# Kernel optimization log

Measured on AMD Instinct MI355X. Metric: run time of the kernel, lower is better.

Reference implementation:

```python
import jax, jax.numpy as jnp
import numpy as np

B, S, C, H, D = 4, 2048, 512, 8, 64
EPS = 1e-5
SCALE = D ** -0.5


def layer_norm(x, w, b):
    m = jnp.mean(x, axis=-1, keepdims=True)
    v = jnp.var(x, axis=-1, keepdims=True)
    return (x - m) * jax.lax.rsqrt(v + EPS) * w + b


def setup_inputs() -> dict:
    key = jax.random.key(0)
    ks = jax.random.split(key, 7)
    s = 0.02
    return {
        "x": jax.random.normal(ks[0], (B, S, C), jnp.float32),
        "Wq": jax.random.normal(ks[1], (C, H * D), jnp.float32) * s,
        "Wk": jax.random.normal(ks[2], (C, H * D), jnp.float32) * s,
        "Wv": jax.random.normal(ks[3], (C, H * D), jnp.float32) * s,
        "Wo": jax.random.normal(ks[4], (H * D, C), jnp.float32) * s,
        "ln1_w": jnp.ones((C,), jnp.float32), "ln1_b": jnp.zeros((C,), jnp.float32),
        "ff_ln1_w": jnp.ones((C,), jnp.float32), "ff_ln1_b": jnp.zeros((C,), jnp.float32),
        "ff_w1": jax.random.normal(ks[5], (C, C), jnp.float32) * s, "ff_b1": jnp.zeros((C,), jnp.float32),
        "ff_ln2_w": jnp.ones((C,), jnp.float32), "ff_ln2_b": jnp.zeros((C,), jnp.float32),
        "ff_w2": jax.random.normal(ks[6], (C, C), jnp.float32) * s, "ff_b2": jnp.zeros((C,), jnp.float32),
        "ln2_w": jnp.ones((C,), jnp.float32), "ln2_b": jnp.zeros((C,), jnp.float32),
    }


def causal_attention(x, Wq, Wk, Wv, Wo):
    # Mathematically identical to the bucketed memory-efficient attention:
    # online-softmax bucketing changes compute order, not the result.
    q = (x @ Wq).reshape(B, S, H, D).transpose(0, 2, 1, 3)  # [B,H,S,D]
    k = (x @ Wk).reshape(B, S, H, D).transpose(0, 2, 1, 3)
    v = (x @ Wv).reshape(B, S, H, D).transpose(0, 2, 1, 3)
    scores = jnp.einsum('bhqd,bhkd->bhqk', q, k) * SCALE  # [B,H,S,S]
    causal = jnp.tril(jnp.ones((S, S), bool))
    scores = jnp.where(causal, scores, jnp.finfo(scores.dtype).min)
    attn = jax.nn.softmax(scores, axis=-1)
    out = jnp.einsum('bhqk,bhkd->bhqd', attn, v)
    out = out.transpose(0, 2, 1, 3).reshape(B, S, H * D)
    return out @ Wo


def reference(x, Wq, Wk, Wv, Wo, ln1_w, ln1_b, ff_ln1_w, ff_ln1_b, ff_w1, ff_b1,
              ff_ln2_w, ff_ln2_b, ff_w2, ff_b2, ln2_w, ln2_b):
    a = causal_attention(x, Wq, Wk, Wv, Wo)
    x_ln = layer_norm(a + x, ln1_w, ln1_b)
    h = layer_norm(x_ln, ff_ln1_w, ff_ln1_b) @ ff_w1 + ff_b1
    h = layer_norm(h, ff_ln2_w, ff_ln2_b) @ ff_w2 + ff_b2
    return layer_norm(h + x_ln, ln2_w, ln2_b)
```

## Files before the change

### kernel.cpp

```cpp
#include <hip/hip_runtime.h>

#define B_ 4
#define S_ 2048
#define C_ 512
#define H_ 8
#define D_ 64
#define M_ 8192

typedef short s8v __attribute__((ext_vector_type(8)));
typedef short s4v __attribute__((ext_vector_type(4)));
typedef float f4v __attribute__((ext_vector_type(4)));
typedef unsigned short u16;
typedef unsigned int u32;
typedef u32 u2v __attribute__((ext_vector_type(2)));

__device__ __forceinline__ u16 f2b(float f) {
    u32 u = __builtin_bit_cast(u32, f);
    u = u + 0x7fffu + ((u >> 16) & 1u);
    return (u16)(u >> 16);
}

__device__ __forceinline__ void b2f8(const s8v v, float* f) {
    #pragma unroll
    for (int k = 0; k < 8; ++k)
        f[k] = __builtin_bit_cast(float, (u32)(u16)v[k] << 16);
}

__device__ __forceinline__ void gl2lds16(const void* g, void* l) {
    __builtin_amdgcn_global_load_lds(
        (const __attribute__((address_space(1))) void*)g,
        (__attribute__((address_space(3))) void*)l, 16, 0, 0);
}

__device__ __forceinline__ s4v pk4(float a, float b, float c, float d) {
    u32 w0, w1;
    asm("v_cvt_pk_bf16_f32 %0, %1, %2" : "=v"(w0) : "v"(a), "v"(b));
    asm("v_cvt_pk_bf16_f32 %0, %1, %2" : "=v"(w1) : "v"(c), "v"(d));
    u2v t; t[0] = w0; t[1] = w1;
    return __builtin_bit_cast(s4v, t);
}

__global__ __launch_bounds__(256) void prep_k(const float* __restrict__ x,
                                              u16* __restrict__ xb,
                                              const float* __restrict__ s0,
                                              const float* __restrict__ s1,
                                              const float* __restrict__ s2,
                                              const float* __restrict__ s3,
                                              const float* __restrict__ s4,
                                              const float* __restrict__ s5,
                                              u16* __restrict__ d0,
                                              u16* __restrict__ d1,
                                              u16* __restrict__ d2,
                                              u16* __restrict__ d3,
                                              u16* __restrict__ d4,
                                              u16* __restrict__ d5)
{
    __shared__ float t[32][33];
    const int bx = blockIdx.x;
    if (bx < 4096) {
        const int i = (bx * 256 + (int)threadIdx.x) * 4;
        const float4 v = *(const float4*)&x[i];
        ushort4 o;
        o.x = f2b(v.x); o.y = f2b(v.y); o.z = f2b(v.z); o.w = f2b(v.w);
        *(ushort4*)&xb[i] = o;
        return;
    }
    const int tb = bx - 4096;
    const int z = tb >> 8, rem = tb & 255;
    const float* W; u16* Wt;
    switch (z) {
        case 0: W = s0; Wt = d0; break;
        case 1: W = s1; Wt = d1; break;
        case 2: W = s2; Wt = d2; break;
        case 3: W = s3; Wt = d3; break;
        case 4: W = s4; Wt = d4; break;
        default: W = s5; Wt = d5; break;
    }
    const int tx = threadIdx.x & 31, ty = threadIdx.x >> 5;
    const int n0 = (rem & 15) * 32, k0 = (rem >> 4) * 32;
    #pragma unroll
    for (int i = 0; i < 4; ++i)
        t[ty + i * 8][tx] = W[(size_t)(k0 + ty + i * 8) * C_ + n0 + tx];
    __syncthreads();
    #pragma unroll
    for (int i = 0; i < 4; ++i)
        Wt[(size_t)(n0 + ty + i * 8) * C_ + k0 + tx] = f2b(t[tx][ty + i * 8]);
}

template <bool OB>
__global__ __launch_bounds__(256) void gemm_k(const u16* __restrict__ A,
                                              const u16* __restrict__ Bt,
                                              const float* __restrict__ bias,
                                              void* __restrict__ outv)
{
    __shared__ u16 As[2][128][64];
    __shared__ u16 Bs[2][64][64];
    const int tid = threadIdx.x;
    const int lane = tid & 63, w = tid >> 6;
    const int q4 = lane >> 4, l16 = lane & 15;
    const int wr = w >> 1, wc = w & 1;
    const int bm = blockIdx.x * 128, bn = blockIdx.y * 64;
    const int sr8  = lane >> 3;
    const int scol = ((lane & 7) ^ sr8) * 8;

    f4v acc[4][2];
    #pragma unroll
    for (int i = 0; i < 4; ++i)
        #pragma unroll
        for (int j = 0; j < 2; ++j) acc[i][j] = (f4v){0.f, 0.f, 0.f, 0.f};

    const u16* Ab = A  + (size_t)bm * C_;
    const u16* Bb = Bt + (size_t)bn * C_;

    auto stage = [&](int bf, int kt) {
        const int k0 = kt * 64;
        #pragma unroll
        for (int t = 0; t < 4; ++t)
            gl2lds16(Ab + (size_t)(w * 32 + t * 8 + sr8) * C_ + k0 + scol,
                     (char*)As + bf * 16384 + (w * 32 + t * 8) * 128);
        #pragma unroll
        for (int t = 0; t < 2; ++t)
            gl2lds16(Bb + (size_t)(w * 16 + t * 8 + sr8) * C_ + k0 + scol,
                     (char*)Bs + bf * 8192 + (w * 16 + t * 8) * 128);
    };

    stage(0, 0);
    for (int kt = 0; kt < 8; ++kt) {
        __syncthreads();
        const int bf = kt & 1;
        if (kt < 7) stage(bf ^ 1, kt + 1);
        #pragma unroll
        for (int kk = 0; kk < 2; ++kk) {
            const int pc = ((kk * 4 + q4) ^ (l16 & 7)) * 8;
            s8v a[4], b[2];
            #pragma unroll
            for (int i = 0; i < 4; ++i)
                a[i] = *(const s8v*)&As[bf][wr * 64 + i * 16 + l16][pc];
            #pragma unroll
            for (int j = 0; j < 2; ++j)
                b[j] = *(const s8v*)&Bs[bf][wc * 32 + j * 16 + l16][pc];
            #pragma unroll
            for (int i = 0; i < 4; ++i)
                #pragma unroll
                for (int j = 0; j < 2; ++j)
                    acc[i][j] = __builtin_amdgcn_mfma_f32_16x16x32_bf16(a[i], b[j], acc[i][j], 0, 0, 0);
        }
    }

    if constexpr (OB) {
        __syncthreads();
        u16* Ls = (u16*)As;
        #pragma unroll
        for (int j = 0; j < 2; ++j) {
            const int nl = wc * 32 + j * 16 + l16;
            const float bj = bias ? bias[bn + nl] : 0.0f;
            #pragma unroll
            for (int i = 0; i < 4; ++i) {
                const int ml = wr * 64 + i * 16 + q4 * 4;
                #pragma unroll
                for (int reg = 0; reg < 4; ++reg)
                    Ls[(ml + reg) * 72 + nl] = f2b(acc[i][j][reg] + bj);
            }
        }
        __syncthreads();
        #pragma unroll
        for (int pass = 0; pass < 4; ++pass) {
            const int idx = tid + pass * 256;
            const int r = idx >> 3, c = idx & 7;
            const s8v v = *(const s8v*)&Ls[r * 72 + c * 8];
            *(s8v*)&((u16*)outv)[(size_t)(bm + r) * C_ + bn + c * 8] = v;
        }
    } else {
        #pragma unroll
        for (int j = 0; j < 2; ++j) {
            const int n = bn + wc * 32 + j * 16 + l16;
            const float bj = bias ? bias[n] : 0.0f;
            #pragma unroll
            for (int i = 0; i < 4; ++i) {
                const int m = bm + wr * 64 + i * 16 + q4 * 4;
                #pragma unroll
                for (int reg = 0; reg < 4; ++reg)
                    ((float*)outv)[(size_t)(m + reg) * C_ + n] = acc[i][j][reg] + bj;
            }
        }
    }
}

__global__ __launch_bounds__(256) void qkv_k(const u16* __restrict__ A,
                                             const u16* __restrict__ Wq,
                                             const u16* __restrict__ Wk,
                                             const u16* __restrict__ Wv,
                                             u16* __restrict__ oq,
                                             u16* __restrict__ ok,
                                             u16* __restrict__ ovt)
{
    __shared__ u16 As[2][128][64];
    __shared__ u16 Bs[2][64][64];
    const int tid = threadIdx.x;
    const int lane = tid & 63, w = tid >> 6;
    const int q4 = lane >> 4, l16 = lane & 15;
    const int wr = w >> 1, wc = w & 1;
    const int nt = blockIdx.y, which = nt >> 3;
    const u16* Bt = which == 0 ? Wq : (which == 1 ? Wk : Wv);
    const int bm = blockIdx.x * 128, bn = (nt & 7) * 64;
    const int sr8  = lane >> 3;
    const int scol = ((lane & 7) ^ sr8) * 8;

    f4v acc[4][2];
    #pragma unroll
    for (int i = 0; i < 4; ++i)
        #pragma unroll
        for (int j = 0; j < 2; ++j) acc[i][j] = (f4v){0.f, 0.f, 0.f, 0.f};

    const u16* Ab = A  + (size_t)bm * C_;
    const u16* Bb = Bt + (size_t)bn * C_;

    auto stage = [&](int bf, int kt) {
        const int k0 = kt * 64;
        #pragma unroll
        for (int t = 0; t < 4; ++t)
            gl2lds16(Ab + (size_t)(w * 32 + t * 8 + sr8) * C_ + k0 + scol,
                     (char*)As + bf * 16384 + (w * 32 + t * 8) * 128);
        #pragma unroll
        for (int t = 0; t < 2; ++t)
            gl2lds16(Bb + (size_t)(w * 16 + t * 8 + sr8) * C_ + k0 + scol,
                     (char*)Bs + bf * 8192 + (w * 16 + t * 8) * 128);
    };

    stage(0, 0);
    for (int kt = 0; kt < 8; ++kt) {
        __syncthreads();
        const int bf = kt & 1;
        if (kt < 7) stage(bf ^ 1, kt + 1);
        #pragma unroll
        for (int kk = 0; kk < 2; ++kk) {
            const int pc = ((kk * 4 + q4) ^ (l16 & 7)) * 8;
            s8v a[4], b[2];
            #pragma unroll
            for (int i = 0; i < 4; ++i)
                a[i] = *(const s8v*)&As[bf][wr * 64 + i * 16 + l16][pc];
            #pragma unroll
            for (int j = 0; j < 2; ++j)
                b[j] = *(const s8v*)&Bs[bf][wc * 32 + j * 16 + l16][pc];
            #pragma unroll
            for (int i = 0; i < 4; ++i)
                #pragma unroll
                for (int j = 0; j < 2; ++j)
                    acc[i][j] = __builtin_amdgcn_mfma_f32_16x16x32_bf16(a[i], b[j], acc[i][j], 0, 0, 0);
        }
    }

    if (which < 2) {
        __syncthreads();
        u16* Ls = (u16*)As;
        #pragma unroll
        for (int j = 0; j < 2; ++j) {
            const int nl = wc * 32 + j * 16 + l16;
            #pragma unroll
            for (int i = 0; i < 4; ++i) {
                const int ml = wr * 64 + i * 16 + q4 * 4;
                #pragma unroll
                for (int reg = 0; reg < 4; ++reg)
                    Ls[(ml + reg) * 72 + nl] = f2b(acc[i][j][reg]);
            }
        }
        __syncthreads();
        u16* dst = which == 0 ? oq : ok;
        #pragma unroll
        for (int pass = 0; pass < 4; ++pass) {
            const int idx = tid + pass * 256;
            const int r = idx >> 3, c = idx & 7;
            const s8v v = *(const s8v*)&Ls[r * 72 + c * 8];
            const int cg = which == 0 ? c : ((c & ~3) | ((c & 3) ^ ((r >> 2) & 3)));
            *(s8v*)&dst[(size_t)(bm + r) * C_ + bn + cg * 8] = v;
        }
    } else {
        const int bglob = bm >> 11;
        const int sbase = bm & (S_ - 1);
        #pragma unroll
        for (int j = 0; j < 2; ++j) {
            const int n = bn + wc * 32 + j * 16 + l16;
            const int h = n >> 6, d = n & 63;
            u16* vrow = ovt + ((size_t)(bglob * H_ + h) * D_ + d) * S_;
            const int xw = d & 7;
            #pragma unroll
            for (int i = 0; i < 4; ++i) {
                const int s = sbase + wr * 64 + i * 16 + q4 * 4;
                const int pg = ((s & 31) >> 2) ^ xw;
                s4v pv;
                #pragma unroll
                for (int reg = 0; reg < 4; ++reg) pv[reg] = (short)f2b(acc[i][j][reg]);
                *(s4v*)&vrow[(s & ~31) + (pg << 2)] = pv;
            }
        }
    }
}

__global__ __launch_bounds__(256) void ln2xb_k(const u16* __restrict__ in,
                                               const float* __restrict__ res,
                                               const float* __restrict__ w1,
                                               const float* __restrict__ b1,
                                               const float* __restrict__ w2,
                                               const float* __restrict__ b2,
                                               u16* __restrict__ out1,
                                               u16* __restrict__ out2)
{
    const int lane = threadIdx.x & 63;
    const int row  = blockIdx.x * 4 + (threadIdx.x >> 6);
    const size_t off = (size_t)row * C_ + lane * 8;
    float v[8];
    b2f8(*(const s8v*)&in[off], v);
    {
        const float4 r0 = *(const float4*)&res[off];
        const float4 r1 = *(const float4*)&res[off + 4];
        v[0] += r0.x; v[1] += r0.y; v[2] += r0.z; v[3] += r0.w;
        v[4] += r1.x; v[5] += r1.y; v[6] += r1.z; v[7] += r1.w;
    }
    float s = 0.f, ss = 0.f;
    #pragma unroll
    for (int k = 0; k < 8; ++k) { s += v[k]; ss += v[k] * v[k]; }
    #pragma unroll
    for (int o = 32; o >= 1; o >>= 1) { s += __shfl_xor(s, o); ss += __shfl_xor(ss, o); }
    float mean = s * (1.0f / C_);
    float rstd = rsqrtf(ss * (1.0f / C_) - mean * mean + 1e-5f);

    const float4 wA0 = *(const float4*)&w1[lane * 8];
    const float4 wA1 = *(const float4*)&w1[lane * 8 + 4];
    const float4 bA0 = *(const float4*)&b1[lane * 8];
    const float4 bA1 = *(const float4*)&b1[lane * 8 + 4];
    const float wA[8] = {wA0.x, wA0.y, wA0.z, wA0.w, wA1.x, wA1.y, wA1.z, wA1.w};
    const float bA[8] = {bA0.x, bA0.y, bA0.z, bA0.w, bA1.x, bA1.y, bA1.z, bA1.w};
    float y[8];
    s8v o1;
    #pragma unroll
    for (int k = 0; k < 8; ++k) {
        y[k] = (v[k] - mean) * rstd * wA[k] + bA[k];
        o1[k] = (short)f2b(y[k]);
    }
    *(s8v*)&out1[off] = o1;

    s = 0.f; ss = 0.f;
    #pragma unroll
    for (int k = 0; k < 8; ++k) { s += y[k]; ss += y[k] * y[k]; }
    #pragma unroll
    for (int o = 32; o >= 1; o >>= 1) { s += __shfl_xor(s, o); ss += __shfl_xor(ss, o); }
    mean = s * (1.0f / C_);
    rstd = rsqrtf(ss * (1.0f / C_) - mean * mean + 1e-5f);

    const float4 wB0 = *(const float4*)&w2[lane * 8];
    const float4 wB1 = *(const float4*)&w2[lane * 8 + 4];
    const float4 bB0 = *(const float4*)&b2[lane * 8];
    const float4 bB1 = *(const float4*)&b2[lane * 8 + 4];
    const float wB[8] = {wB0.x, wB0.y, wB0.z, wB0.w, wB1.x, wB1.y, wB1.z, wB1.w};
    const float bB[8] = {bB0.x, bB0.y, bB0.z, bB0.w, bB1.x, bB1.y, bB1.z, bB1.w};
    s8v o2;
    #pragma unroll
    for (int k = 0; k < 8; ++k)
        o2[k] = (short)f2b((y[k] - mean) * rstd * wB[k] + bB[k]);
    *(s8v*)&out2[off] = o2;
}

__global__ __launch_bounds__(256) void lnb_k(const u16* __restrict__ in,
                                             const float* __restrict__ w,
                                             const float* __restrict__ bb,
                                             u16* __restrict__ out)
{
    const int lane = threadIdx.x & 63;
    const int row  = blockIdx.x * 4 + (threadIdx.x >> 6);
    const size_t off = (size_t)row * C_ + lane * 8;
    float v[8];
    b2f8(*(const s8v*)&in[off], v);
    float s = 0.f, ss = 0.f;
    #pragma unroll
    for (int k = 0; k < 8; ++k) { s += v[k]; ss += v[k] * v[k]; }
    #pragma unroll
    for (int o = 32; o >= 1; o >>= 1) { s += __shfl_xor(s, o); ss += __shfl_xor(ss, o); }
    const float mean = s * (1.0f / C_);
    const float rstd = rsqrtf(ss * (1.0f / C_) - mean * mean + 1e-5f);
    const float4 w0 = *(const float4*)&w[lane * 8];
    const float4 w1 = *(const float4*)&w[lane * 8 + 4];
    const float4 b0 = *(const float4*)&bb[lane * 8];
    const float4 b1 = *(const float4*)&bb[lane * 8 + 4];
    const float wv[8] = {w0.x, w0.y, w0.z, w0.w, w1.x, w1.y, w1.z, w1.w};
    const float bv[8] = {b0.x, b0.y, b0.z, b0.w, b1.x, b1.y, b1.z, b1.w};
    s8v o;
    #pragma unroll
    for (int k = 0; k < 8; ++k)
        o[k] = (short)f2b((v[k] - mean) * rstd * wv[k] + bv[k]);
    *(s8v*)&out[off] = o;
}

__global__ __launch_bounds__(256) void lnfin_k(const u16* __restrict__ in,
                                               const u16* __restrict__ res,
                                               const float* __restrict__ w,
                                               const float* __restrict__ bb,
                                               float* __restrict__ out)
{
    const int lane = threadIdx.x & 63;
    const int row  = blockIdx.x * 4 + (threadIdx.x >> 6);
    const size_t off = (size_t)row * C_ + lane * 8;
    float v[8], r[8];
    b2f8(*(const s8v*)&in[off], v);
    b2f8(*(const s8v*)&res[off], r);
    #pragma unroll
    for (int k = 0; k < 8; ++k) v[k] += r[k];
    float s = 0.f, ss = 0.f;
    #pragma unroll
    for (int k = 0; k < 8; ++k) { s += v[k]; ss += v[k] * v[k]; }
    #pragma unroll
    for (int o = 32; o >= 1; o >>= 1) { s += __shfl_xor(s, o); ss += __shfl_xor(ss, o); }
    const float mean = s * (1.0f / C_);
    const float rstd = rsqrtf(ss * (1.0f / C_) - mean * mean + 1e-5f);
    const float4 w0 = *(const float4*)&w[lane * 8];
    const float4 w1 = *(const float4*)&w[lane * 8 + 4];
    const float4 b0 = *(const float4*)&bb[lane * 8];
    const float4 b1 = *(const float4*)&bb[lane * 8 + 4];
    const float wv[8] = {w0.x, w0.y, w0.z, w0.w, w1.x, w1.y, w1.z, w1.w};
    const float bv[8] = {b0.x, b0.y, b0.z, b0.w, b1.x, b1.y, b1.z, b1.w};
    float4 o0, o1;
    o0.x = (v[0] - mean) * rstd * wv[0] + bv[0];
    o0.y = (v[1] - mean) * rstd * wv[1] + bv[1];
    o0.z = (v[2] - mean) * rstd * wv[2] + bv[2];
    o0.w = (v[3] - mean) * rstd * wv[3] + bv[3];
    o1.x = (v[4] - mean) * rstd * wv[4] + bv[4];
    o1.y = (v[5] - mean) * rstd * wv[5] + bv[5];
    o1.z = (v[6] - mean) * rstd * wv[6] + bv[6];
    o1.w = (v[7] - mean) * rstd * wv[7] + bv[7];
    *(float4*)&out[off]     = o0;
    *(float4*)&out[off + 4] = o1;
}

__global__ __launch_bounds__(512, 4) void attn_k(const u16* __restrict__ Q,
                                                 const u16* __restrict__ K,
                                                 const u16* __restrict__ Vt,
                                                 u16* __restrict__ O)
{
    __shared__ char smem[65536];
    u16* KsB = (u16*)smem;
    u16* VsB = (u16*)(smem + 32768);
    const int tid = threadIdx.x;
    const int lane = tid & 63, w = tid >> 6;
    const int grp = w >> 2, wl = w & 3;
    const int q4 = lane >> 4, l16 = lane & 15;
    const int h = blockIdx.x, px = blockIdx.y, b = blockIdx.z;
    const int qH = 31 - px, qL = px;
    const int nH = 32 - px;
    const size_t base  = ((size_t)b * S_) * C_ + h * D_;
    const size_t basev = ((size_t)(b * H_ + h)) * D_ * S_;
    const int lr = lane >> 2, lc = (lane & 3) * 8;
    const int kq = (q4 ^ ((l16 >> 2) & 3)) * 8;
    const int qrow = wl * 16 + l16;

    const u16* ksA = KsB + grp * 4096;
    const u16* ksBp = KsB + (grp + 2) * 4096;
    const u16* vsA = VsB + grp * 4096;
    const u16* vsBp = VsB + (grp + 2) * 4096;
    char* kdA = (char*)KsB + grp * 8192 + wl * 1024;
    char* kdB = (char*)KsB + (grp + 2) * 8192 + wl * 1024;
    char* vdA = (char*)VsB + grp * 8192 + wl * 1024;
    char* vdB = (char*)VsB + (grp + 2) * 8192 + wl * 1024;

    const int kfb = l16 * 32 + kq;
    int vfb[4];
    #pragma unroll
    for (int c = 0; c < 4; ++c)
        vfb[c] = l16 * 32 + ((((c & 1) * 4 + q4) ^ (l16 & 7)) * 4);

    const u16* kpt = K  + base  + (size_t)(wl * 16 + lr) * C_ + lc;
    const u16* vpt = Vt + basev + (size_t)(wl * 16 + lr) * S_ + lc;

    f4v acc[4]; float lp[4];
    f4v oH[4];  float lpH[4];
    #pragma unroll
    for (int j = 0; j < 4; ++j) {
        acc[j] = (f4v){0.f, 0.f, 0.f, 0.f}; lp[j] = 0.f;
        oH[j]  = (f4v){0.f, 0.f, 0.f, 0.f}; lpH[j] = 0.f;
    }
    s8v qf[2];
    #pragma unroll
    for (int kh = 0; kh < 2; ++kh)
        qf[kh] = *(const s8v*)&Q[base + (size_t)(qH * 64 + qrow) * C_ + kh * 32 + q4 * 8];

    bool dumped = false, wrapped = false;

    auto dumpacc = [&]() {
        #pragma unroll
        for (int j = 0; j < 4; ++j) {
            oH[j] = acc[j]; lpH[j] = lp[j];
            acc[j] = (f4v){0.f, 0.f, 0.f, 0.f}; lp[j] = 0.f;
        }
        #pragma unroll
        for (int kh = 0; kh < 2; ++kh)
            qf[kh] = *(const s8v*)&Q[base + (size_t)(qL * 64 + qrow) * C_ + kh * 32 + q4 * 8];
    };

    auto compute = [&](const u16* ks, const u16* vs, const bool diag) {
        f4v sc[4];
        #pragma unroll
        for (int j = 0; j < 4; ++j) sc[j] = (f4v){0.f, 0.f, 0.f, 0.f};
        __builtin_amdgcn_s_setprio(1);
        #pragma unroll
        for (int kh = 0; kh < 2; ++kh)
            #pragma unroll
            for (int j = 0; j < 4; ++j) {
                const s8v kf = *(const s8v*)&ks[kfb + kh * 2048 + j * 512];
                sc[j] = __builtin_amdgcn_mfma_f32_16x16x32_bf16(kf, qf[kh], sc[j], 0, 0, 0);
            }
        __builtin_amdgcn_s_setprio(0);
        s4v pa[4];
        if (diag) {
            #pragma unroll
            for (int j = 0; j < 4; ++j) {
                float pv[4];
                #pragma unroll
                for (int reg = 0; reg < 4; ++reg) {
                    float tt = fmaf(sc[j][reg], 0.18033688011112043f, -11.541560327111707f);
                    if ((j * 16 + q4 * 4 + reg) > qrow) tt = -128.0f;
                    pv[reg] = exp2f(tt);
                }
                lp[j] += (pv[0] + pv[1]) + (pv[2] + pv[3]);
                pa[j] = pk4(pv[0], pv[1], pv[2], pv[3]);
            }
        } else {
            #pragma unroll
            for (int j = 0; j < 4; ++j) {
                float pv[4];
                #pragma unroll
                for (int reg = 0; reg < 4; ++reg)
                    pv[reg] = exp2f(fmaf(sc[j][reg], 0.18033688011112043f,
                                         -11.541560327111707f));
                lp[j] += (pv[0] + pv[1]) + (pv[2] + pv[3]);
                pa[j] = pk4(pv[0], pv[1], pv[2], pv[3]);
            }
        }
        __builtin_amdgcn_s_setprio(1);
        #pragma unroll
        for (int c = 0; c < 4; ++c)
            #pragma unroll
            for (int dj = 0; dj < 4; ++dj) {
                const s4v vb = *(const s4v*)&vs[vfb[c] + (c >> 1) * 2048 + dj * 512];
                acc[dj] = __builtin_amdgcn_mfma_f32_16x16x16bf16_1k(pa[c], vb, acc[dj], 0, 0, 0);
            }
        __builtin_amdgcn_s_setprio(0);
    };

    {
        const u16* kc = kpt + (size_t)(grp * 64) * C_;
        const u16* vc = vpt + grp * 64;
        gl2lds16(kc, kdA); gl2lds16(kc + 32, kdA + 4096);
        gl2lds16(vc, vdA); gl2lds16(vc + 32, vdA + 4096);
    }
    const u16* kcur = kpt + (size_t)((grp + 2) * 64) * C_;
    const u16* vcur = vpt + (grp + 2) * 64;
    int snext = grp + 2;
    int s = grp;

    auto advance = [&]() {
        kcur += (size_t)128 * C_;
        vcur += 128;
        snext += 2;
        if (!wrapped && snext >= nH) {
            kcur -= (size_t)(nH * 64) * C_;
            vcur -= nH * 64;
            wrapped = true;
        }
    };

    for (int u = 0; u < 8; ++u) {
        __syncthreads();
        {
            gl2lds16(kcur, kdB); gl2lds16(kcur + 32, kdB + 4096);
            gl2lds16(vcur, vdB); gl2lds16(vcur + 32, vdB + 4096);
            advance();
        }
        if (!dumped && s >= nH) { dumped = true; dumpacc(); }
        compute(ksA, vsA, (s == nH - 1) || (s == 32));
        s += 2;
        __syncthreads();
        if (u < 7 || grp == 0) {
            gl2lds16(kcur, kdA); gl2lds16(kcur + 32, kdA + 4096);
            gl2lds16(vcur, vdA); gl2lds16(vcur + 32, vdA + 4096);
            advance();
        }
        if (!dumped && s >= nH) { dumped = true; dumpacc(); }
        compute(ksBp, vsBp, (s == nH - 1) || (s == 32));
        s += 2;
    }
    __syncthreads();
    if (grp == 0) {
        if (!dumped) { dumped = true; dumpacc(); }
        compute(ksA, vsA, true);
    }
    if (!dumped) {
        #pragma unroll
        for (int j = 0; j < 4; ++j) {
            oH[j] = acc[j]; lpH[j] = lp[j];
            acc[j] = (f4v){0.f, 0.f, 0.f, 0.f}; lp[j] = 0.f;
        }
    }

    __syncthreads();
    float* exH = (float*)smem;
    float* exL = (float*)(smem + 20480);
    {
        float* p = (grp ? exH : exL) + (wl * 64 + lane) * 20;
        if (grp) {
            #pragma unroll
            for (int dj = 0; dj < 4; ++dj)
                #pragma unroll
                for (int reg = 0; reg < 4; ++reg) p[dj * 4 + reg] = oH[dj][reg];
            #pragma unroll
            for (int j = 0; j < 4; ++j) p[16 + j] = lpH[j];
        } else {
            #pragma unroll
            for (int dj = 0; dj < 4; ++dj)
                #pragma unroll
                for (int reg = 0; reg < 4; ++reg) p[dj * 4 + reg] = acc[dj][reg];
            #pragma unroll
            for (int j = 0; j < 4; ++j) p[16 + j] = lp[j];
        }
    }
    __syncthreads();
    if (grp == 0) {
        const float* p = exH + (wl * 64 + lane) * 20;
        #pragma unroll
        for (int dj = 0; dj < 4; ++dj)
            #pragma unroll
            for (int reg = 0; reg < 4; ++reg) oH[dj][reg] += p[dj * 4 + reg];
        #pragma unroll
        for (int j = 0; j < 4; ++j) lpH[j] += p[16 + j];
        float lt = (lpH[0] + lpH[1]) + (lpH[2] + lpH[3]);
        lt += __shfl_xor(lt, 16);
        lt += __shfl_xor(lt, 32);
        #pragma unroll
        for (int reg = 0; reg < 4; ++reg) {
            const float inv = 1.0f / __shfl(lt, q4 * 4 + reg);
            const size_t rowoff = base + (size_t)(qH * 64 + wl * 16 + q4 * 4 + reg) * C_;
            #pragma unroll
            for (int dj = 0; dj < 4; ++dj)
                O[rowoff + dj * 16 + l16] = f2b(oH[dj][reg] * inv);
        }
    } else {
        const float* p = exL + (wl * 64 + lane) * 20;
        #pragma unroll
        for (int dj = 0; dj < 4; ++dj)
            #pragma unroll
            for (int reg = 0; reg < 4; ++reg) acc[dj][reg] += p[dj * 4 + reg];
        #pragma unroll
        for (int j = 0; j < 4; ++j) lp[j] += p[16 + j];
        float lt = (lp[0] + lp[1]) + (lp[2] + lp[3]);
        lt += __shfl_xor(lt, 16);
        lt += __shfl_xor(lt, 32);
        #pragma unroll
        for (int reg = 0; reg < 4; ++reg) {
            const float inv = 1.0f / __shfl(lt, q4 * 4 + reg);
            const size_t rowoff = base + (size_t)(qL * 64 + wl * 16 + q4 * 4 + reg) * C_;
            #pragma unroll
            for (int dj = 0; dj < 4; ++dj)
                O[rowoff + dj * 16 + l16] = f2b(acc[dj][reg] * inv);
        }
    }
}

extern "C" void kernel_launch(void* const* d_in, const int* in_sizes, int n_in,
                              void* d_out, int out_size, void* d_ws, size_t ws_size,
                              hipStream_t stream)
{
    const float* x       = (const float*)d_in[0];
    const float* Wq      = (const float*)d_in[1];
    const float* Wk      = (const float*)d_in[2];
    const float* Wv      = (const float*)d_in[3];
    const float* Wo      = (const float*)d_in[4];
    const float* ln1_w   = (const float*)d_in[5];
    const float* ln1_b   = (const float*)d_in[6];
    const float* ffln1_w = (const float*)d_in[7];
    const float* ffln1_b = (const float*)d_in[8];
    const float* ff_w1   = (const float*)d_in[9];
    const float* ff_b1   = (const float*)d_in[10];
    const float* ffln2_w = (const float*)d_in[11];
    const float* ffln2_b = (const float*)d_in[12];
    const float* ff_w2   = (const float*)d_in[13];
    const float* ff_b2   = (const float*)d_in[14];
    const float* ln2_w   = (const float*)d_in[15];
    const float* ln2_b   = (const float*)d_in[16];
    float* out = (float*)d_out;

    const size_t MC = (size_t)M_ * C_;
    const size_t WW = (size_t)C_ * C_;
    u16* xb   = (u16*)d_ws;
    u16* WqT  = xb + MC;
    u16* WkT  = WqT + WW;
    u16* WvT  = WkT + WW;
    u16* WoT  = WvT + WW;
    u16* W1T  = WoT + WW;
    u16* W2T  = W1T + WW;
    u16* qbuf = W2T + WW;
    u16* kbuf = qbuf + MC;
    u16* vbuf = kbuf + MC;
    u16* vtbuf= vbuf + MC;
    u16*  abuf = xb;
    u16*  tf   = qbuf;
    u16*  xln  = vbuf;

    const dim3 gg(M_ / 128, C_ / 64);
    const dim3 gq(M_ / 128, 24);
    const dim3 ga(H_, 16, B_);
    const int  gl = M_ / 4;

    prep_k<<<5632, 256, 0, stream>>>(x, xb, Wq, Wk, Wv, Wo, ff_w1, ff_w2,
                                     WqT, WkT, WvT, WoT, W1T, W2T);

    qkv_k<<<gq, 256, 0, stream>>>(xb, WqT, WkT, WvT, qbuf, kbuf, vtbuf);
    attn_k<<<ga, 512, 0, stream>>>(qbuf, kbuf, vtbuf, abuf);

    gemm_k<true><<<gg, 256, 0, stream>>>(abuf, WoT, nullptr, tf);
    ln2xb_k<<<gl, 256, 0, stream>>>(tf, x, ln1_w, ln1_b, ffln1_w, ffln1_b,
                                    xln, xb);
    gemm_k<true><<<gg, 256, 0, stream>>>(xb, W1T, ff_b1, tf);
    lnb_k<<<gl, 256, 0, stream>>>(tf, ffln2_w, ffln2_b, xb);
    gemm_k<true><<<gg, 256, 0, stream>>>(xb, W2T, ff_b2, tf);
    lnfin_k<<<gl, 256, 0, stream>>>(tf, xln, ln2_w, ln2_b, out);
}
```

Before: 220.1 us.

## Widen QKV GEMM tile to 128x128 with 512 threads; truncate P to bf16

The QKV projection kernel moves from 128x64 tiles on 256 threads to 128x128 tiles on 512 threads. This halves the grid and raises reuse of the A tile staged in shared memory. The epilogue uses a wider padded LDS buffer to match. Separately, the attention softmax drops the packed round-to-nearest bf16 convert in favour of plain truncation of the upper 16 bits, accumulating the row sum inline. Truncation saves convert instructions but adds a small rounding bias in P.

```diff
diff --git a/kernel.cpp b/kernel.cpp
--- a/kernel.cpp
+++ b/kernel.cpp
@@ -12,7 +12,6 @@
 typedef float f4v __attribute__((ext_vector_type(4)));
 typedef unsigned short u16;
 typedef unsigned int u32;
-typedef u32 u2v __attribute__((ext_vector_type(2)));
 
 __device__ __forceinline__ u16 f2b(float f) {
     u32 u = __builtin_bit_cast(u32, f);
@@ -30,14 +29,6 @@
     __builtin_amdgcn_global_load_lds(
         (const __attribute__((address_space(1))) void*)g,
         (__attribute__((address_space(3))) void*)l, 16, 0, 0);
-}
-
-__device__ __forceinline__ s4v pk4(float a, float b, float c, float d) {
-    u32 w0, w1;
-    asm("v_cvt_pk_bf16_f32 %0, %1, %2" : "=v"(w0) : "v"(a), "v"(b));
-    asm("v_cvt_pk_bf16_f32 %0, %1, %2" : "=v"(w1) : "v"(c), "v"(d));
-    u2v t; t[0] = w0; t[1] = w1;
-    return __builtin_bit_cast(s4v, t);
 }
 
 __global__ __launch_bounds__(256) void prep_k(const float* __restrict__ x,
@@ -186,7 +177,7 @@
     }
 }
 
-__global__ __launch_bounds__(256) void qkv_k(const u16* __restrict__ A,
+__global__ __launch_bounds__(512) void qkv_k(const u16* __restrict__ A,
                                              const u16* __restrict__ Wq,
                                              const u16* __restrict__ Wk,
                                              const u16* __restrict__ Wv,
@@ -195,14 +186,14 @@
                                              u16* __restrict__ ovt)
 {
     __shared__ u16 As[2][128][64];
-    __shared__ u16 Bs[2][64][64];
+    __shared__ u16 Bs[2][128][64];
     const int tid = threadIdx.x;
     const int lane = tid & 63, w = tid >> 6;
     const int q4 = lane >> 4, l16 = lane & 15;
-    const int wr = w >> 1, wc = w & 1;
-    const int nt = blockIdx.y, which = nt >> 3;
+    const int wr = w >> 2, wc = w & 3;
+    const int nt = blockIdx.y, which = nt >> 2;
     const u16* Bt = which == 0 ? Wq : (which == 1 ? Wk : Wv);
-    const int bm = blockIdx.x * 128, bn = (nt & 7) * 64;
+    const int bm = blockIdx.x * 128, bn = (nt & 3) * 128;
     const int sr8  = lane >> 3;
     const int scol = ((lane & 7) ^ sr8) * 8;
 
@@ -218,13 +209,12 @@
     auto stage = [&](int bf, int kt) {
         const int k0 = kt * 64;
         #pragma unroll
-        for (int t = 0; t < 4; ++t)
-            gl2lds16(Ab + (size_t)(w * 32 + t * 8 + sr8) * C_ + k0 + scol,
-                     (char*)As + bf * 16384 + (w * 32 + t * 8) * 128);
-        #pragma unroll
-        for (int t = 0; t < 2; ++t)
+        for (int t = 0; t < 2; ++t) {
+            gl2lds16(Ab + (size_t)(w * 16 + t * 8 + sr8) * C_ + k0 + scol,
+                     (char*)As + bf * 16384 + (w * 16 + t * 8) * 128);
             gl2lds16(Bb + (size_t)(w * 16 + t * 8 + sr8) * C_ + k0 + scol,
-                     (char*)Bs + bf * 8192 + (w * 16 + t * 8) * 128);
+                     (char*)Bs + bf * 16384 + (w * 16 + t * 8) * 128);
+        }
     };
 
     stage(0, 0);
@@ -261,16 +251,16 @@
                 const int ml = wr * 64 + i * 16 + q4 * 4;
                 #pragma unroll
                 for (int reg = 0; reg < 4; ++reg)
-                    Ls[(ml + reg) * 72 + nl] = f2b(acc[i][j][reg]);
+                    Ls[(ml + reg) * 132 + nl] = f2b(acc[i][j][reg]);
             }
         }
         __syncthreads();
         u16* dst = which == 0 ? oq : ok;
         #pragma unroll
         for (int pass = 0; pass < 4; ++pass) {
-            const int idx = tid + pass * 256;
-            const int r = idx >> 3, c = idx & 7;
-            const s8v v = *(const s8v*)&Ls[r * 72 + c * 8];
+            const int idx = tid + pass * 512;
+            const int r = idx >> 4, c = idx & 15;
+            const s8v v = *(const s8v*)&Ls[r * 132 + c * 8];
             const int cg = which == 0 ? c : ((c & ~3) | ((c & 3) ^ ((r >> 2) & 3)));
             *(s8v*)&dst[(size_t)(bm + r) * C_ + bn + cg * 8] = v;
         }
@@ -511,26 +501,29 @@
         if (diag) {
             #pragma unroll
             for (int j = 0; j < 4; ++j) {
-                float pv[4];
+                float ps = 0.0f;
                 #pragma unroll
                 for (int reg = 0; reg < 4; ++reg) {
                     float tt = fmaf(sc[j][reg], 0.18033688011112043f, -11.541560327111707f);
                     if ((j * 16 + q4 * 4 + reg) > qrow) tt = -128.0f;
-                    pv[reg] = exp2f(tt);
+                    const float p = exp2f(tt);
+                    ps += p;
+                    pa[j][reg] = (short)(__builtin_bit_cast(u32, p) >> 16);
                 }
-                lp[j] += (pv[0] + pv[1]) + (pv[2] + pv[3]);
-                pa[j] = pk4(pv[0], pv[1], pv[2], pv[3]);
+                lp[j] += ps;
             }
         } else {
             #pragma unroll
             for (int j = 0; j < 4; ++j) {
-                float pv[4];
-                #pragma unroll
-                for (int reg = 0; reg < 4; ++reg)
-                    pv[reg] = exp2f(fmaf(sc[j][reg], 0.18033688011112043f,
-                                         -11.541560327111707f));
-                lp[j] += (pv[0] + pv[1]) + (pv[2] + pv[3]);
-                pa[j] = pk4(pv[0], pv[1], pv[2], pv[3]);
+                float ps = 0.0f;
+                #pragma unroll
+                for (int reg = 0; reg < 4; ++reg) {
+                    const float p = exp2f(fmaf(sc[j][reg], 0.18033688011112043f,
+                                               -11.541560327111707f));
+                    ps += p;
+                    pa[j][reg] = (short)(__builtin_bit_cast(u32, p) >> 16);
+                }
+                lp[j] += ps;
             }
         }
         __builtin_amdgcn_s_setprio(1);
@@ -703,14 +696,14 @@
     u16*  xln  = vbuf;
 
     const dim3 gg(M_ / 128, C_ / 64);
-    const dim3 gq(M_ / 128, 24);
+    const dim3 gq(M_ / 128, 12);
     const dim3 ga(H_, 16, B_);
     const int  gl = M_ / 4;
 
     prep_k<<<5632, 256, 0, stream>>>(x, xb, Wq, Wk, Wv, Wo, ff_w1, ff_w2,
                                      WqT, WkT, WvT, WoT, W1T, W2T);
 
-    qkv_k<<<gq, 256, 0, stream>>>(xb, WqT, WkT, WvT, qbuf, kbuf, vtbuf);
+    qkv_k<<<gq, 512, 0, stream>>>(xb, WqT, WkT, WvT, qbuf, kbuf, vtbuf);
     attn_k<<<ga, 512, 0, stream>>>(qbuf, kbuf, vtbuf, abuf);
 
     gemm_k<true><<<gg, 256, 0, stream>>>(abuf, WoT, nullptr, tf);
```

Result: no change. 221.0 us (+0.4%).
